# Performance work log

Hardware: AMD Instinct MI355X
Metric: run time of the kernel (lower is better)

The kernel has to match this reference:

```python
import jax, jax.numpy as jnp
import numpy as np

B, ME, R, N, HSZ, V, L, NHEADS = 32, 384, 128, 512, 500, 1000, 2, 4


def _ln(x, g, b, eps=1e-5):
    mu = jnp.mean(x, axis=-1, keepdims=True)
    var = jnp.mean((x - mu) ** 2, axis=-1, keepdims=True)
    return (x - mu) / jnp.sqrt(var + eps) * g + b


def setup_inputs() -> dict:
    key = jax.random.key(0)
    ks = jax.random.split(key, 12)
    ent_vec = jax.random.normal(ks[0], (B, ME, HSZ), jnp.float32)
    entity_num = jax.random.randint(ks[1], (B,), 1, ME + 1)
    rels = jax.random.randint(ks[2], (B, R), 0, V)
    sizes = entity_num + R  # real graph size per sample (<= N)
    idx = jnp.arange(N)
    valid = idx[None, :] < sizes[:, None]
    adj = jax.random.uniform(ks[3], (B, N, N)) < 0.3
    adj = adj & valid[:, None, :] & valid[:, :, None]
    adj = adj | jnp.eye(N, dtype=bool)[None]  # keep diagonal so no all-masked row
    adj = adj.astype(jnp.int32)
    rel_embed = jax.random.normal(ks[4], (V, HSZ)) * (2.0 / (V + HSZ)) ** 0.5  # xavier_normal

    def w(k, shape):
        return (jax.random.normal(k, shape) * 0.03).astype(jnp.float32)

    Wq = w(ks[5], (L, HSZ, HSZ)); Wk = w(ks[6], (L, HSZ, HSZ))
    Wv = w(ks[7], (L, HSZ, HSZ)); Wo = w(ks[8], (L, HSZ, HSZ))
    W1 = w(ks[9], (L, HSZ, 4 * HSZ)); W2 = w(ks[10], (L, 4 * HSZ, HSZ))
    zH = jnp.zeros((L, HSZ), jnp.float32)
    return dict(
        ent_vec=ent_vec, entity_num=entity_num, rels=rels, adj=adj,
        rel_embed=rel_embed,
        Wq=Wq, bq=zH, Wk=Wk, bk=zH, Wv=Wv, bv=zH, Wo=Wo, bo=zH,
        W1=W1, b1=jnp.zeros((L, 4 * HSZ), jnp.float32), W2=W2, b2=zH,
        ln1_g=jnp.ones((L, HSZ), jnp.float32), ln1_b=zH,
        ln2_g=jnp.ones((L, HSZ), jnp.float32), ln2_b=zH,
        prelu_a=jnp.full((L, 4 * HSZ), 0.25, jnp.float32),
    )


def reference(ent_vec, entity_num, rels, adj, rel_embed,
              Wq, bq, Wk, bk, Wv, bv, Wo, bo,
              W1, b1, W2, b2, ln1_g, ln1_b, ln2_g, ln2_b, prelu_a):
    Bb, Me, H = ent_vec.shape
    Rr = rels.shape[1]
    Nn = adj.shape[1]
    Ll = Wq.shape[0]
    dh = H // NHEADS
    idx = jnp.arange(Nn)

    # query_graph = concat(ent_vec[i][:entity_num[i]], rel_embed(rels[i])), padded to N
    is_ent = idx[None, :] < entity_num[:, None]
    eidx = jnp.minimum(idx[None, :], Me - 1)
    ent_part = jnp.take_along_axis(ent_vec, eidx[:, :, None], axis=1)  # (B,N,H)
    ridx = jnp.clip(idx[None, :] - entity_num[:, None], 0, Rr - 1)
    rel_ids = jnp.take_along_axis(rels, ridx, axis=1)  # (B,N)
    rel_part = rel_embed[rel_ids]  # (B,N,H)
    nodes = jnp.where(is_ent[:, :, None], ent_part, rel_part)
    sizes = entity_num + Rr
    validm = idx[None, :] < sizes[:, None]
    nodes = nodes * validm[:, :, None]

    attn_mask = adj != 0  # original masks where adj == 0
    scale = 1.0 / jnp.sqrt(jnp.float32(dh))
    for l in range(Ll):
        kv = jax.lax.stop_gradient(nodes)  # key_graph is detached in original
        q = (nodes @ Wq[l] + bq[l]).reshape(Bb, Nn, NHEADS, dh)
        k = (kv @ Wk[l] + bk[l]).reshape(Bb, Nn, NHEADS, dh)
        v = (kv @ Wv[l] + bv[l]).reshape(Bb, Nn, NHEADS, dh)
        s = jnp.einsum('bqhd,bkhd->bhqk', q, k) * scale
        s = jnp.where(attn_mask[:, None], s, jnp.float32(-1e9))
        a = jax.nn.softmax(s, axis=-1)
        ctx = jnp.einsum('bhqk,bkhd->bqhd', a, v).reshape(Bb, Nn, H)
        o = ctx @ Wo[l] + bo[l]
        t = _ln(o, ln1_g[l], ln1_b[l])
        h1 = t @ W1[l] + b1[l]
        h1 = jnp.where(h1 > 0, h1, prelu_a[l] * h1)  # PReLU, per-channel
        f = h1 @ W2[l] + b2[l]
        nodes = _ln(f + t, ln2_g[l], ln2_b[l])

    node_emb = nodes * validm[:, :, None]  # original pads graphs with zeros
    gidx = jnp.broadcast_to(entity_num[:, None, None], (Bb, 1, H))
    glob = jnp.take_along_axis(nodes, gidx, axis=1)[:, 0]  # query_graph[entity_num[i]]
    out_mask = idx[None, :] <= sizes[:, None]  # faithful '<=' as in original
    return glob, node_emb, out_mask
```

## Files before the change

kernel.cpp:

```cpp
#include <hip/hip_runtime.h>

#define BB 32
#define MEE 384
#define RRELS 128
#define NNODES 512
#define HSZ 500
#define DHEAD 125
#define NHEADS_ 4
#define HID 2000
#define NLAYER 2

#define KP 512
#define HIDP 2048

typedef unsigned short ushort_t;
typedef __attribute__((ext_vector_type(8))) short bf16x8;
typedef __attribute__((ext_vector_type(4))) float f32x4;
typedef __attribute__((ext_vector_type(4))) short s16x4;

static __device__ __forceinline__ unsigned short f2bf(float x) {
    unsigned u = __float_as_uint(x);
    u = u + 0x7fff + ((u >> 16) & 1);
    return (unsigned short)(u >> 16);
}
static __device__ __forceinline__ float bf2f(unsigned short b) {
    return __uint_as_float((unsigned)b << 16);
}

static __device__ __forceinline__ void gload_lds16(const ushort_t* g, ushort_t* l) {
    __builtin_amdgcn_global_load_lds(
        (const __attribute__((address_space(1))) void*)g,
        (__attribute__((address_space(3))) void*)l, 16, 0, 0);
}

__global__ __launch_bounds__(256) void build_nodes_k(
    const float* __restrict__ ent_vec, const int* __restrict__ entity_num,
    const int* __restrict__ rels, const float* __restrict__ rel_embed,
    ushort_t* __restrict__ xb)
{
    int b = blockIdx.x / NNODES;
    int n = blockIdx.x % NNODES;
    int e = entity_num[b];
    const float* src = nullptr;
    if (n < e)               src = ent_vec + ((size_t)b * MEE + n) * HSZ;
    else if (n < e + RRELS)  src = rel_embed + (size_t)rels[b * RRELS + (n - e)] * HSZ;
    ushort_t* xd = xb + ((size_t)b * NNODES + n) * KP;
    for (int d = threadIdx.x; d < KP; d += 256)
        xd[d] = (src && d < HSZ) ? f2bf(src[d]) : 0;
}

__global__ __launch_bounds__(256) void adj_bits_k(
    const int* __restrict__ adj, unsigned int* __restrict__ bits)
{
    int gw = (blockIdx.x * 256 + threadIdx.x) >> 6;
    int lane = threadIdx.x & 63;
    int v = adj[(size_t)gw * 64 + lane];
    unsigned long long mk = __ballot(v != 0);
    if (lane == 0)  bits[gw * 2]     = (unsigned int)mk;
    if (lane == 32) bits[gw * 2 + 1] = (unsigned int)(mk >> 32);
}

__global__ __launch_bounds__(256) void wcvt_t_k(
    const float* __restrict__ pWq, const float* __restrict__ pWk,
    const float* __restrict__ pWv, const float* __restrict__ pWo,
    const float* __restrict__ pW1, const float* __restrict__ pW2,
    ushort_t* __restrict__ wqkv, ushort_t* __restrict__ wo,
    ushort_t* __restrict__ w1, ushort_t* __restrict__ w2)
{
    __shared__ float T[64][65];
    int blk = blockIdx.x;
    const float* W; ushort_t* out; int Kr, Nr, Kpp, tt;
    if (blk < 192)      { int s = blk >> 6; W = s == 0 ? pWq : (s == 1 ? pWk : pWv);
                          out = wqkv + s * 262144; Kr = 500; Nr = 500; Kpp = 512; tt = blk & 63; }
    else if (blk < 256) { W = pWo; out = wo;  Kr = 500;  Nr = 500;  Kpp = 512;  tt = blk - 192; }
    else if (blk < 512) { W = pW1; out = w1;  Kr = 500;  Nr = 2000; Kpp = 512;  tt = blk - 256; }
    else                { W = pW2; out = w2;  Kr = 2000; Nr = 500;  Kpp = 2048; tt = blk - 512; }
    int ntk = Kpp >> 6;
    int tk = tt % ntk, tn = tt / ntk;
    int tid = threadIdx.x;
#pragma unroll
    for (int p = 0; p < 4; ++p) {
        int kl = p * 16 + (tid >> 4);
        int k  = tk * 64 + kl;
        int nl = (tid & 15) * 4;
        int n  = tn * 64 + nl;
        float4 v = make_float4(0.f, 0.f, 0.f, 0.f);
        if (k < Kr) {
            if (n + 3 < Nr) v = *(const float4*)&W[(size_t)k * Nr + n];
            else {
                if (n     < Nr) v.x = W[(size_t)k * Nr + n];
                if (n + 1 < Nr) v.y = W[(size_t)k * Nr + n + 1];
                if (n + 2 < Nr) v.z = W[(size_t)k * Nr + n + 2];
                if (n + 3 < Nr) v.w = W[(size_t)k * Nr + n + 3];
            }
        }
        T[kl][nl] = v.x; T[kl][nl + 1] = v.y; T[kl][nl + 2] = v.z; T[kl][nl + 3] = v.w;
    }
    __syncthreads();
#pragma unroll
    for (int p = 0; p < 2; ++p) {
        int nl  = p * 32 + (tid >> 3);
        int kl8 = (tid & 7) * 8;
        bf16x8 o;
#pragma unroll
        for (int j = 0; j < 8; ++j) o[j] = (short)f2bf(T[kl8 + j][nl]);
        *(bf16x8*)&out[(size_t)(tn * 64 + nl) * Kpp + tk * 64 + kl8] = o;
    }
}

__global__ __launch_bounds__(256, 2) void gemm_mfma_k(
    const ushort_t* __restrict__ A, const ushort_t* __restrict__ Bt,
    const float* __restrict__ bias0, const float* __restrict__ bias1,
    const float* __restrict__ bias2,
    ushort_t* __restrict__ outB, ushort_t* __restrict__ outK,
    ushort_t* __restrict__ outV,
    int M, int Np, int Kp, int Nreal,
    const float* __restrict__ prelu, int mode)
{
    __shared__ ushort_t Al[2][128 * 32];
    __shared__ ushort_t Bl[2][128 * 32];

    const int nwg = gridDim.x * gridDim.y;
    const int bid = blockIdx.y * gridDim.x + blockIdx.x;
    const int swz = (bid & 7) * (nwg >> 3) + (bid >> 3);
    const int bm = (swz / gridDim.x) * 128;
    const int bn = (swz % gridDim.x) * 128;

    const int tid = threadIdx.x;
    const int wid = tid >> 6, lane = tid & 63;
    const int wr = wid >> 1, wc = wid & 1;
    const int lr = lane & 15, lk = lane >> 4;

    f32x4 acc[4][4];
#pragma unroll
    for (int i = 0; i < 4; ++i)
#pragma unroll
        for (int j = 0; j < 4; ++j)
#pragma unroll
            for (int r = 0; r < 4; ++r) acc[i][j][r] = 0.f;

    const int srow = tid >> 2;
    const int skseg = (tid & 3) * 8;
    const ushort_t* Ag0 = A + (size_t)(bm + srow) * Kp + skseg;
    const ushort_t* Ag1 = A + (size_t)(bm + 64 + srow) * Kp + skseg;
    const ushort_t* Bg0 = Bt + (size_t)(bn + srow) * Kp + skseg;
    const ushort_t* Bg1 = Bt + (size_t)(bn + 64 + srow) * Kp + skseg;

    auto stage = [&](int bi, int k0) {
        gload_lds16(Ag0 + k0, &Al[bi][wid * 512]);
        gload_lds16(Ag1 + k0, &Al[bi][2048 + wid * 512]);
        gload_lds16(Bg0 + k0, &Bl[bi][wid * 512]);
        gload_lds16(Bg1 + k0, &Bl[bi][2048 + wid * 512]);
    };

    stage(0, 0);
    __syncthreads();
    int cur = 0;

    for (int k0 = 0; k0 < Kp; k0 += 32) {
        if (k0 + 32 < Kp) stage(cur ^ 1, k0 + 32);

        bf16x8 af[4], bfr[4];
#pragma unroll
        for (int mi = 0; mi < 4; ++mi)
            af[mi] = *(const bf16x8*)&Al[cur][(wr * 64 + mi * 16 + lr) * 32 + lk * 8];
#pragma unroll
        for (int ni = 0; ni < 4; ++ni)
            bfr[ni] = *(const bf16x8*)&Bl[cur][(wc * 64 + ni * 16 + lr) * 32 + lk * 8];
        __builtin_amdgcn_s_setprio(1);
#pragma unroll
        for (int mi = 0; mi < 4; ++mi)
#pragma unroll
            for (int ni = 0; ni < 4; ++ni)
                acc[mi][ni] = __builtin_amdgcn_mfma_f32_16x16x32_bf16(
                    af[mi], bfr[ni], acc[mi][ni], 0, 0, 0);
        __builtin_amdgcn_s_setprio(0);

        __syncthreads();
        cur ^= 1;
    }

    if (mode == 1) {
#pragma unroll
        for (int ni = 0; ni < 4; ++ni) {
            int col = bn + wc * 64 + ni * 16 + lr;
            int reg = col >> 9, c = col & 511;
            bool cok = c < 500;
            int hh, dh;
            if (cok) { hh = c / 125; dh = c - hh * 125; }
            else     { hh = (c - 500) / 3; dh = 125 + (c - 500) % 3; }
            const float* bp = reg == 0 ? bias0 : (reg == 1 ? bias1 : bias2);
            float bv = cok ? bp[c] : 0.f;
#pragma unroll
            for (int mi = 0; mi < 4; ++mi) {
                int row0 = bm + wr * 64 + mi * 16 + lk * 4;
                int b_ = row0 >> 9, n0 = row0 & 511;
                size_t bh = (size_t)b_ * 4 + hh;
                if (reg == 2) {
                    s16x4 pk;
#pragma unroll
                    for (int r = 0; r < 4; ++r) {
                        float val = acc[mi][ni][r] + bv;
                        pk[r] = cok ? (short)f2bf(val) : (short)0;
                    }
                    *(s16x4*)&outV[(bh * 128 + dh) * 512 + n0] = pk;
                } else {
                    ushort_t* dst = reg == 0 ? outB : outK;
#pragma unroll
                    for (int r = 0; r < 4; ++r) {
                        float val = acc[mi][ni][r] + bv;
                        dst[(bh * 512 + n0 + r) * 128 + dh] = cok ? f2bf(val) : 0;
                    }
                }
            }
        }
    } else {
#pragma unroll
        for (int ni = 0; ni < 4; ++ni) {
            int col = bn + wc * 64 + ni * 16 + lr;
            bool cok = col < Nreal;
            float bv = cok ? bias0[col] : 0.f;
            float pv = (prelu && cok) ? prelu[col] : 0.f;
#pragma unroll
            for (int mi = 0; mi < 4; ++mi) {
                int row0 = bm + wr * 64 + mi * 16 + lk * 4;
#pragma unroll
                for (int r = 0; r < 4; ++r) {
                    int row = row0 + r;
                    float val = acc[mi][ni][r] + bv;
                    if (prelu) val = val > 0.f ? val : pv * val;
                    outB[(size_t)row * Np + col] = cok ? f2bf(val) : 0;
                }
            }
        }
    }
}

#define KTT 64
__global__ __launch_bounds__(256, 2) void attn_mfma_k(
    const ushort_t* __restrict__ qh, const ushort_t* __restrict__ kh,
    const ushort_t* __restrict__ vT, const unsigned int* __restrict__ abits,
    ushort_t* __restrict__ ctxb)
{
    __shared__ ushort_t Kl[2][KTT * 128];
    __shared__ ushort_t Vl[2][128 * KTT];
    __shared__ ushort_t Pl[4][32 * KTT];

    const int bid = blockIdx.x;
    const int wg = (bid & 7) * 64 + (bid >> 3);
    const int qt2 = wg & 3, bh = wg >> 2;
    const int b = bh >> 2, h = bh & 3;
    const int tid = threadIdx.x, wid = tid >> 6, lane = tid & 63;
    const int lr = lane & 15, lk = lane >> 4;
    const int q0 = qt2 * 128 + wid * 32;
    const float scale2 = 0.08944271909999159f * 1.44269504088896f;

    bf16x8 qa[2][4];
#pragma unroll
    for (int t = 0; t < 2; ++t) {
        const ushort_t* qbase = qh + ((size_t)bh * 512 + q0 + t * 16 + lr) * 128;
#pragma unroll
        for (int ks = 0; ks < 4; ++ks)
            qa[t][ks] = *(const bf16x8*)&qbase[ks * 32 + lk * 8];
    }

    f32x4 accO[2][8];
#pragma unroll
    for (int t = 0; t < 2; ++t)
#pragma unroll
        for (int i = 0; i < 8; ++i)
#pragma unroll
            for (int r = 0; r < 4; ++r) accO[t][i][r] = 0.f;
    float m_[2][4], l_[2][4];
#pragma unroll
    for (int t = 0; t < 2; ++t)
#pragma unroll
        for (int r = 0; r < 4; ++r) { m_[t][r] = -3e38f; l_[t][r] = 0.f; }

    const unsigned int* ab = abits + ((size_t)b * NNODES + q0) * 16;

    auto stage = [&](int bi, int kt) {
#pragma unroll
        for (int i = 0; i < 4; ++i) {
            int linear = (wid * 4 + i) * 64 + lane;
            int row = linear >> 4, cc = linear & 15;
            int cs = cc ^ (row & 7);
            gload_lds16(kh + ((size_t)bh * 512 + kt * 64 + row) * 128 + cs * 8,
                        &Kl[bi][(wid * 4 + i) * 512]);
        }
#pragma unroll
        for (int i = 0; i < 4; ++i) {
            int linear = (wid * 4 + i) * 64 + lane;
            int row = linear >> 3, cc = linear & 7;
            int cs = cc ^ (row & 7);
            gload_lds16(vT + ((size_t)bh * 128 + row) * 512 + kt * 64 + cs * 8,
                        &Vl[bi][(wid * 4 + i) * 512]);
        }
    };

    stage(0, 0);
    __syncthreads();
    int cur = 0;

    for (int kt = 0; kt < NNODES / KTT; ++kt) {
        if (kt < NNODES / KTT - 1) stage(cur ^ 1, kt + 1);

        unsigned int mw[2][4][2];
#pragma unroll
        for (int t = 0; t < 2; ++t)
#pragma unroll
            for (int r = 0; r < 4; ++r) {
                int qrow = t * 16 + lk * 4 + r;
                mw[t][r][0] = ab[qrow * 16 + kt * 2];
                mw[t][r][1] = ab[qrow * 16 + kt * 2 + 1];
            }

#pragma unroll
        for (int t = 0; t < 2; ++t) {
            f32x4 accS[4];
#pragma unroll
            for (int ni = 0; ni < 4; ++ni)
#pragma unroll
                for (int r = 0; r < 4; ++r) accS[ni][r] = 0.f;
            __builtin_amdgcn_s_setprio(1);
#pragma unroll
            for (int ks = 0; ks < 4; ++ks) {
#pragma unroll
                for (int ni = 0; ni < 4; ++ni) {
                    int row = ni * 16 + lr;
                    int ch = (ks * 4 + lk) ^ (row & 7);
                    bf16x8 kb = *(const bf16x8*)&Kl[cur][row * 128 + ch * 8];
                    accS[ni] = __builtin_amdgcn_mfma_f32_16x16x32_bf16(
                        qa[t][ks], kb, accS[ni], 0, 0, 0);
                }
            }
            __builtin_amdgcn_s_setprio(0);

            float s_all[4][4], mnew[4];
#pragma unroll
            for (int r = 0; r < 4; ++r) {
                float rowmax = -3e38f;
#pragma unroll
                for (int ni = 0; ni < 4; ++ni) {
                    unsigned int word = mw[t][r][ni >> 1];
                    int bit = (ni & 1) * 16 + lr;
                    bool on = (word >> bit) & 1u;
                    float sv = on ? accS[ni][r] * scale2 : -1e9f;
                    s_all[r][ni] = sv;
                    rowmax = fmaxf(rowmax, sv);
                }
                rowmax = fmaxf(rowmax, __shfl_xor(rowmax, 1));
                rowmax = fmaxf(rowmax, __shfl_xor(rowmax, 2));
                rowmax = fmaxf(rowmax, __shfl_xor(rowmax, 4));
                rowmax = fmaxf(rowmax, __shfl_xor(rowmax, 8));
                mnew[r] = fmaxf(m_[t][r], rowmax);
            }
            bool need = false;
#pragma unroll
            for (int r = 0; r < 4; ++r) need = need || (mnew[r] - m_[t][r] > 8.f);
            if (__any(need)) {
#pragma unroll
                for (int r = 0; r < 4; ++r) {
                    float f = exp2f(m_[t][r] - mnew[r]);
                    m_[t][r] = mnew[r];
                    l_[t][r] *= f;
#pragma unroll
                    for (int di = 0; di < 8; ++di) accO[t][di][r] *= f;
                }
            }
#pragma unroll
            for (int r = 0; r < 4; ++r) {
                float p[4], rs = 0.f;
#pragma unroll
                for (int ni = 0; ni < 4; ++ni) {
                    p[ni] = exp2f(s_all[r][ni] - m_[t][r]);
                    rs += p[ni];
                }
                rs += __shfl_xor(rs, 1);
                rs += __shfl_xor(rs, 2);
                rs += __shfl_xor(rs, 4);
                rs += __shfl_xor(rs, 8);
                l_[t][r] += rs;
                int q = t * 16 + lk * 4 + r;
#pragma unroll
                for (int ni = 0; ni < 4; ++ni) {
                    int key = ni * 16 + lr;
                    Pl[wid][q * 64 + (((key >> 3) ^ (q & 7)) << 3) + (key & 7)] = f2bf(p[ni]);
                }
            }
        }

#pragma unroll
        for (int t = 0; t < 2; ++t) {
#pragma unroll
            for (int ksp = 0; ksp < 2; ++ksp) {
                int q = t * 16 + lr;
                int k0p = ksp * 32 + lk * 8;
                bf16x8 pa = *(const bf16x8*)&Pl[wid][q * 64 + (((k0p >> 3) ^ (q & 7)) << 3)];
                __builtin_amdgcn_s_setprio(1);
#pragma unroll
                for (int di = 0; di < 8; ++di) {
                    int row = di * 16 + lr;
                    int ch = (ksp * 4 + lk) ^ (row & 7);
                    bf16x8 vb = *(const bf16x8*)&Vl[cur][row * 64 + ch * 8];
                    accO[t][di] = __builtin_amdgcn_mfma_f32_16x16x32_bf16(
                        pa, vb, accO[t][di], 0, 0, 0);
                }
                __builtin_amdgcn_s_setprio(0);
            }
        }
        __syncthreads();
        cur ^= 1;
    }

    float inv[2][4];
#pragma unroll
    for (int t = 0; t < 2; ++t)
#pragma unroll
        for (int r = 0; r < 4; ++r) inv[t][r] = 1.f / l_[t][r];
#pragma unroll
    for (int t = 0; t < 2; ++t)
#pragma unroll
        for (int di = 0; di < 8; ++di) {
            int d = di * 16 + lr;
            if (d < DHEAD) {
#pragma unroll
                for (int r = 0; r < 4; ++r) {
                    int qg = q0 + t * 16 + lk * 4 + r;
                    ctxb[((size_t)b * NNODES + qg) * KP + h * DHEAD + d] =
                        f2bf(accO[t][di][r] * inv[t][r]);
                }
            }
        }
    if (h == 3) {
        int row = q0 + (lane & 31);
        int c0 = 500 + (lane >> 5) * 6;
#pragma unroll
        for (int j = 0; j < 6; ++j)
            ctxb[((size_t)b * NNODES + row) * KP + c0 + j] = 0;
    }
}

__global__ __launch_bounds__(256) void ln_k(
    const ushort_t* __restrict__ x, const ushort_t* __restrict__ res,
    const float* __restrict__ g, const float* __restrict__ bta,
    ushort_t* __restrict__ outB,
    const int* __restrict__ entity_num, float* __restrict__ out, int final_)
{
    size_t row = blockIdx.x;
    const unsigned int* xr = (const unsigned int*)(x + row * KP);
    const unsigned int* rr = res ? (const unsigned int*)(res + row * KP) : nullptr;
    int t = threadIdx.x;
    int d0 = 2 * t;
    unsigned int xv = xr[t];
    float v0 = bf2f((unsigned short)(xv & 0xffff));
    float v1 = bf2f((unsigned short)(xv >> 16));
    if (rr) {
        unsigned int rv = rr[t];
        v0 += bf2f((unsigned short)(rv & 0xffff));
        v1 += bf2f((unsigned short)(rv >> 16));
    }
    if (d0 >= HSZ) v0 = 0.f;
    if (d0 + 1 >= HSZ) v1 = 0.f;
    float s = v0 + v1, s2 = v0 * v0 + v1 * v1;

    __shared__ float red[8];
    int wave = t >> 6, lane = t & 63;
    for (int o = 1; o < 64; o <<= 1) { s += __shfl_xor(s, o); s2 += __shfl_xor(s2, o); }
    if (lane == 0) { red[wave] = s; red[4 + wave] = s2; }
    __syncthreads();
    s  = red[0] + red[1] + red[2] + red[3];
    s2 = red[4] + red[5] + red[6] + red[7];
    float mean = s / HSZ;
    float var  = s2 / HSZ - mean * mean;
    float rstd = rsqrtf(var + 1e-5f);

    float o0 = 0.f, o1 = 0.f;
    if (d0 < HSZ)     o0 = (v0 - mean) * rstd * g[d0] + bta[d0];
    if (d0 + 1 < HSZ) o1 = (v1 - mean) * rstd * g[d0 + 1] + bta[d0 + 1];

    if (!final_) {
        unsigned int pk = (unsigned int)f2bf(o0) | ((unsigned int)f2bf(o1) << 16);
        if (d0 >= HSZ) pk = 0;
        else if (d0 + 1 >= HSZ) pk = (unsigned int)f2bf(o0);
        ((unsigned int*)(outB + row * KP))[t] = pk;
    } else {
        int b = (int)(row >> 9), n = (int)(row & 511);
        int e = entity_num[b];
        int size = e + RRELS;
        bool valid = n < size;
        float* ne = out + (size_t)BB * HSZ + row * HSZ;
        if (d0 < HSZ)     ne[d0]     = valid ? o0 : 0.f;
        if (d0 + 1 < HSZ) ne[d0 + 1] = valid ? o1 : 0.f;
        if (n == e) {
            float* gl = out + (size_t)b * HSZ;
            if (d0 < HSZ)     gl[d0]     = o0;
            if (d0 + 1 < HSZ) gl[d0 + 1] = o1;
        }
        if (t == 0)
            out[(size_t)BB * HSZ + (size_t)BB * NNODES * HSZ + row] =
                (n <= size) ? 1.f : 0.f;
    }
}

extern "C" void kernel_launch(void* const* d_in, const int* in_sizes, int n_in,
                              void* d_out, int out_size, void* d_ws, size_t ws_size,
                              hipStream_t stream)
{
    const float* ent_vec    = (const float*)d_in[0];
    const int*   entity_num = (const int*)d_in[1];
    const int*   rels       = (const int*)d_in[2];
    const int*   adj        = (const int*)d_in[3];
    const float* rel_embed  = (const float*)d_in[4];
    const float* Wq = (const float*)d_in[5],  *bq = (const float*)d_in[6];
    const float* Wk = (const float*)d_in[7],  *bk = (const float*)d_in[8];
    const float* Wv = (const float*)d_in[9],  *bv = (const float*)d_in[10];
    const float* Wo = (const float*)d_in[11], *bo = (const float*)d_in[12];
    const float* W1 = (const float*)d_in[13], *b1 = (const float*)d_in[14];
    const float* W2 = (const float*)d_in[15], *b2 = (const float*)d_in[16];
    const float* ln1g = (const float*)d_in[17], *ln1b = (const float*)d_in[18];
    const float* ln2g = (const float*)d_in[19], *ln2b = (const float*)d_in[20];
    const float* pa = (const float*)d_in[21];

    const int M = BB * NNODES;
    const size_t SP = (size_t)M * KP;

    ushort_t* Xb   = (ushort_t*)d_ws;
    ushort_t* ctxb = Xb + SP;
    ushort_t* tb   = ctxb + SP;
    ushort_t* ob   = tb + SP;
    ushort_t* fb   = ob + SP;
    ushort_t* h1b  = fb + SP;
    ushort_t* wqkvb = h1b + (size_t)M * HIDP;
    ushort_t* wob  = wqkvb + 3 * KP * KP;
    ushort_t* w1b  = wob + KP * KP;
    ushort_t* w2b  = w1b + (size_t)HIDP * KP;

    ushort_t* qh  = h1b;
    ushort_t* kh  = h1b + SP;
    ushort_t* vTb = h1b + 2 * SP;

    unsigned int* abits = (unsigned int*)d_out;

    build_nodes_k<<<BB * NNODES, 256, 0, stream>>>(ent_vec, entity_num, rels, rel_embed, Xb);
    adj_bits_k<<<(BB * NNODES * NNODES) / 64 / 4, 256, 0, stream>>>(adj, abits);

    for (int l = 0; l < NLAYER; ++l) {
        const float* bq_l = bq + (size_t)l * HSZ;
        const float* bk_l = bk + (size_t)l * HSZ;
        const float* bv_l = bv + (size_t)l * HSZ;
        const float* bo_l = bo + (size_t)l * HSZ;
        const float* b1_l = b1 + (size_t)l * HID;
        const float* b2_l = b2 + (size_t)l * HSZ;
        const float* pa_l = pa + (size_t)l * HID;

        wcvt_t_k<<<768, 256, 0, stream>>>(
            Wq + (size_t)l * HSZ * HSZ, Wk + (size_t)l * HSZ * HSZ,
            Wv + (size_t)l * HSZ * HSZ, Wo + (size_t)l * HSZ * HSZ,
            W1 + (size_t)l * HSZ * HID, W2 + (size_t)l * HID * HSZ,
            wqkvb, wob, w1b, w2b);

        dim3 gQKV(1536 / 128, M / 128);
        gemm_mfma_k<<<gQKV, 256, 0, stream>>>(Xb, wqkvb, bq_l, bk_l, bv_l,
                                              qh, kh, vTb,
                                              M, 1536, KP, HSZ, nullptr, 1);

        attn_mfma_k<<<BB * NHEADS_ * 4, 256, 0, stream>>>(qh, kh, vTb, abits, ctxb);

        dim3 gO(KP / 128, M / 128);
        gemm_mfma_k<<<gO, 256, 0, stream>>>(ctxb, wob, bo_l, nullptr, nullptr,
                                            ob, nullptr, nullptr,
                                            M, KP, KP, HSZ, nullptr, 0);
        ln_k<<<M, 256, 0, stream>>>(ob, nullptr,
                                    ln1g + (size_t)l * HSZ, ln1b + (size_t)l * HSZ,
                                    tb, nullptr, nullptr, 0);

        dim3 g1(HIDP / 128, M / 128);
        gemm_mfma_k<<<g1, 256, 0, stream>>>(tb, w1b, b1_l, nullptr, nullptr,
                                            h1b, nullptr, nullptr,
                                            M, HIDP, KP, HID, pa_l, 0);
        dim3 g2(KP / 128, M / 128);
        gemm_mfma_k<<<g2, 256, 0, stream>>>(h1b, w2b, b2_l, nullptr, nullptr,
                                            fb, nullptr, nullptr,
                                            M, KP, HIDP, HSZ, nullptr, 0);

        int fin = (l == NLAYER - 1) ? 1 : 0;
        ln_k<<<M, 256, 0, stream>>>(fb, tb,
                                    ln2g + (size_t)l * HSZ, ln2b + (size_t)l * HSZ,
                                    Xb, entity_num, (float*)d_out, fin);
    }
}
```

Baseline: 529.0 us.

## Triple-buffer GEMM LDS pipeline and convert both layers' weights in one launch

The GEMM kernel moves from double to triple-buffered LDS staging with explicit vmcnt waits and raw barriers, keeping two tiles in flight ahead of compute. It also raises the occupancy hint to 3 blocks per CU. Weight conversion for both layers now runs in a single launch before the layer loop, which removes one kernel launch. The cost is more LDS per block (48KB) and a larger workspace holding both layers' bf16 weights.

```diff
diff --git a/kernel.cpp b/kernel.cpp
--- a/kernel.cpp
+++ b/kernel.cpp
@@ -68,13 +68,24 @@
     ushort_t* __restrict__ w1, ushort_t* __restrict__ w2)
 {
     __shared__ float T[64][65];
-    int blk = blockIdx.x;
+    int blk0 = blockIdx.x;
+    int layer = blk0 >> 9 >= 1 && blk0 >= 768 ? 1 : 0;
+    layer = blk0 / 768;
+    int blk = blk0 - layer * 768;
     const float* W; ushort_t* out; int Kr, Nr, Kpp, tt;
-    if (blk < 192)      { int s = blk >> 6; W = s == 0 ? pWq : (s == 1 ? pWk : pWv);
-                          out = wqkv + s * 262144; Kr = 500; Nr = 500; Kpp = 512; tt = blk & 63; }
-    else if (blk < 256) { W = pWo; out = wo;  Kr = 500;  Nr = 500;  Kpp = 512;  tt = blk - 192; }
-    else if (blk < 512) { W = pW1; out = w1;  Kr = 500;  Nr = 2000; Kpp = 512;  tt = blk - 256; }
-    else                { W = pW2; out = w2;  Kr = 2000; Nr = 500;  Kpp = 2048; tt = blk - 512; }
+    if (blk < 192)      { int s = blk >> 6;
+                          W = (s == 0 ? pWq : (s == 1 ? pWk : pWv)) + (size_t)layer * HSZ * HSZ;
+                          out = wqkv + (size_t)layer * 786432 + s * 262144;
+                          Kr = 500; Nr = 500; Kpp = 512; tt = blk & 63; }
+    else if (blk < 256) { W = pWo + (size_t)layer * HSZ * HSZ;
+                          out = wo + (size_t)layer * 262144;
+                          Kr = 500;  Nr = 500;  Kpp = 512;  tt = blk - 192; }
+    else if (blk < 512) { W = pW1 + (size_t)layer * HSZ * HID;
+                          out = w1 + (size_t)layer * 1048576;
+                          Kr = 500;  Nr = 2000; Kpp = 512;  tt = blk - 256; }
+    else                { W = pW2 + (size_t)layer * HID * HSZ;
+                          out = w2 + (size_t)layer * 1048576;
+                          Kr = 2000; Nr = 500;  Kpp = 2048; tt = blk - 512; }
     int ntk = Kpp >> 6;
     int tk = tt % ntk, tn = tt / ntk;
     int tid = threadIdx.x;
@@ -108,7 +119,7 @@
     }
 }
 
-__global__ __launch_bounds__(256, 2) void gemm_mfma_k(
+__global__ __launch_bounds__(256, 3) void gemm_mfma_k(
     const ushort_t* __restrict__ A, const ushort_t* __restrict__ Bt,
     const float* __restrict__ bias0, const float* __restrict__ bias1,
     const float* __restrict__ bias2,
@@ -117,8 +128,8 @@
     int M, int Np, int Kp, int Nreal,
     const float* __restrict__ prelu, int mode)
 {
-    __shared__ ushort_t Al[2][128 * 32];
-    __shared__ ushort_t Bl[2][128 * 32];
+    __shared__ ushort_t Al[3][128 * 32];
+    __shared__ ushort_t Bl[3][128 * 32];
 
     const int nwg = gridDim.x * gridDim.y;
     const int bid = blockIdx.y * gridDim.x + blockIdx.x;
@@ -153,13 +164,17 @@
         gload_lds16(Bg1 + k0, &Bl[bi][2048 + wid * 512]);
     };
 
+    const int nstep = Kp >> 5;
+
     stage(0, 0);
-    __syncthreads();
+    stage(1, 32);
+    stage(2, 64);
+    asm volatile("s_waitcnt vmcnt(8)" ::: "memory");
+    __builtin_amdgcn_s_barrier();
+    __builtin_amdgcn_sched_barrier(0);
+
     int cur = 0;
-
-    for (int k0 = 0; k0 < Kp; k0 += 32) {
-        if (k0 + 32 < Kp) stage(cur ^ 1, k0 + 32);
-
+    for (int t = 0; t < nstep; ++t) {
         bf16x8 af[4], bfr[4];
 #pragma unroll
         for (int mi = 0; mi < 4; ++mi)
@@ -176,8 +191,25 @@
                     af[mi], bfr[ni], acc[mi][ni], 0, 0, 0);
         __builtin_amdgcn_s_setprio(0);
 
-        __syncthreads();
-        cur ^= 1;
+        if (t == nstep - 1) break;
+
+        __builtin_amdgcn_sched_barrier(0);
+        __builtin_amdgcn_s_barrier();
+        __builtin_amdgcn_sched_barrier(0);
+
+        if (t + 3 < nstep) {
+            stage(cur, (t + 3) * 32);
+            asm volatile("s_waitcnt vmcnt(8)" ::: "memory");
+        } else if (t + 3 == nstep) {
+            asm volatile("s_waitcnt vmcnt(4)" ::: "memory");
+        } else {
+            asm volatile("s_waitcnt vmcnt(0)" ::: "memory");
+        }
+        __builtin_amdgcn_sched_barrier(0);
+        __builtin_amdgcn_s_barrier();
+        __builtin_amdgcn_sched_barrier(0);
+
+        cur = cur + 1; if (cur == 3) cur = 0;
     }
 
     if (mode == 1) {
@@ -532,9 +564,9 @@
     ushort_t* fb   = ob + SP;
     ushort_t* h1b  = fb + SP;
     ushort_t* wqkvb = h1b + (size_t)M * HIDP;
-    ushort_t* wob  = wqkvb + 3 * KP * KP;
-    ushort_t* w1b  = wob + KP * KP;
-    ushort_t* w2b  = w1b + (size_t)HIDP * KP;
+    ushort_t* wob  = wqkvb + 2 * 786432;
+    ushort_t* w1b  = wob + 2 * 262144;
+    ushort_t* w2b  = w1b + 2 * (size_t)1048576;
 
     ushort_t* qh  = h1b;
     ushort_t* kh  = h1b + SP;
@@ -544,6 +576,7 @@
 
     build_nodes_k<<<BB * NNODES, 256, 0, stream>>>(ent_vec, entity_num, rels, rel_embed, Xb);
     adj_bits_k<<<(BB * NNODES * NNODES) / 64 / 4, 256, 0, stream>>>(adj, abits);
+    wcvt_t_k<<<1536, 256, 0, stream>>>(Wq, Wk, Wv, Wo, W1, W2, wqkvb, wob, w1b, w2b);
 
     for (int l = 0; l < NLAYER; ++l) {
         const float* bq_l = bq + (size_t)l * HSZ;
@@ -553,22 +586,20 @@
         const float* b1_l = b1 + (size_t)l * HID;
         const float* b2_l = b2 + (size_t)l * HSZ;
         const float* pa_l = pa + (size_t)l * HID;
-
-        wcvt_t_k<<<768, 256, 0, stream>>>(
-            Wq + (size_t)l * HSZ * HSZ, Wk + (size_t)l * HSZ * HSZ,
-            Wv + (size_t)l * HSZ * HSZ, Wo + (size_t)l * HSZ * HSZ,
-            W1 + (size_t)l * HSZ * HID, W2 + (size_t)l * HID * HSZ,
-            wqkvb, wob, w1b, w2b);
+        ushort_t* wqkv_l = wqkvb + (size_t)l * 786432;
+        ushort_t* wo_l   = wob  + (size_t)l * 262144;
+        ushort_t* w1_l   = w1b  + (size_t)l * 1048576;
+        ushort_t* w2_l   = w2b  + (size_t)l * 1048576;
 
         dim3 gQKV(1536 / 128, M / 128);
-        gemm_mfma_k<<<gQKV, 256, 0, stream>>>(Xb, wqkvb, bq_l, bk_l, bv_l,
+        gemm_mfma_k<<<gQKV, 256, 0, stream>>>(Xb, wqkv_l, bq_l, bk_l, bv_l,
                                               qh, kh, vTb,
                                               M, 1536, KP, HSZ, nullptr, 1);
 
         attn_mfma_k<<<BB * NHEADS_ * 4, 256, 0, stream>>>(qh, kh, vTb, abits, ctxb);
 
         dim3 gO(KP / 128, M / 128);
-        gemm_mfma_k<<<gO, 256, 0, stream>>>(ctxb, wob, bo_l, nullptr, nullptr,
+        gemm_mfma_k<<<gO, 256, 0, stream>>>(ctxb, wo_l, bo_l, nullptr, nullptr,
                                             ob, nullptr, nullptr,
                                             M, KP, KP, HSZ, nullptr, 0);
         ln_k<<<M, 256, 0, stream>>>(ob, nullptr,
@@ -576,11 +607,11 @@
                                     tb, nullptr, nullptr, 0);
 
         dim3 g1(HIDP / 128, M / 128);
-        gemm_mfma_k<<<g1, 256, 0, stream>>>(tb, w1b, b1_l, nullptr, nullptr,
+        gemm_mfma_k<<<g1, 256, 0, stream>>>(tb, w1_l, b1_l, nullptr, nullptr,
                                             h1b, nullptr, nullptr,
                                             M, HIDP, KP, HID, pa_l, 0);
         dim3 g2(KP / 128, M / 128);
-        gemm_mfma_k<<<g2, 256, 0, stream>>>(h1b, w2b, b2_l, nullptr, nullptr,
+        gemm_mfma_k<<<g2, 256, 0, stream>>>(h1b, w2_l, b2_l, nullptr, nullptr,
                                             fb, nullptr, nullptr,
                                             M, KP, HIDP, HSZ, nullptr, 0);
 
```

Measured after the change: 524.4 us. About the same (-0.9%).
